# Kernel optimization log

Measured on AMD Instinct MI355X. Metric: run time of the kernel, lower is better.

Reference implementation:

```python
import jax, jax.numpy as jnp
import numpy as np

D = 256
B, S, N = 4, 512, 4


def setup_inputs() -> dict:
    key = jax.random.key(0)
    ks = jax.random.split(key, 24)
    d, dq = D, D // 4
    std = 0.02
    inp = {
        'x':   jax.random.normal(ks[0], (B, S, N, d), jnp.float32),
        'Wq':  jax.random.normal(ks[1], (d, d), jnp.float32) * std,
        'Wk':  jax.random.normal(ks[2], (d, d), jnp.float32) * std,
        'Wv':  jax.random.normal(ks[3], (d, d), jnp.float32) * std,
        'Wg1': jax.random.normal(ks[4], (d, d), jnp.float32) * std,
        'bg1': jnp.zeros((d,), jnp.float32),
        'Wg2': jax.random.normal(ks[5], (d, d), jnp.float32) * std,
        'bg2': jnp.zeros((d,), jnp.float32),
        'We1': jax.random.normal(ks[6], (d, dq), jnp.float32) * std,
        'be1': jnp.zeros((dq,), jnp.float32),
        'We2': jax.random.normal(ks[7], (dq, 1), jnp.float32) * std,
        'be2': jnp.zeros((1,), jnp.float32),
        'Wa1': jax.random.normal(ks[8], (d, dq), jnp.float32) * std,
        'ba1': jnp.zeros((dq,), jnp.float32),
        'Wa2': jax.random.normal(ks[9], (dq, 1), jnp.float32) * std,
        'ba2': jnp.zeros((1,), jnp.float32),
        'Wo':  jax.random.normal(ks[10], (d, d), jnp.float32) * std,
        'bo':  jnp.zeros((d,), jnp.float32),
        'gamma': jnp.ones((d,), jnp.float32),
        'beta':  jnp.zeros((d,), jnp.float32),
    }
    return inp


def reference(x, Wq, Wk, Wv, Wg1, bg1, Wg2, bg2, We1, be1, We2, be2,
              Wa1, ba1, Wa2, ba2, Wo, bo, gamma, beta):
    b, s, n, f = x.shape
    xf = x.reshape(b * n, s, f)  # matches torch .view on contiguous x
    residual = xf

    q = xf @ Wq                                    # [bn, s, d]
    k = xf @ Wk
    v = xf @ Wv
    v_hat = jax.nn.silu(v @ Wg1 + bg1) @ Wg2 + bg2  # value_generator
    eta = jax.nn.sigmoid(jax.nn.silu(xf @ We1 + be1) @ We2 + be2) * 0.1 + 0.01   # [bn, s, 1]
    alpha = jax.nn.sigmoid(jax.nn.silu(xf @ Wa1 + ba1) @ Wa2 + ba2) * 0.5 + 0.5  # [bn, s, 1]

    # F.normalize(k, dim=-1): eps = 1e-12
    kn = k / jnp.maximum(jnp.linalg.norm(k, axis=-1, keepdims=True), 1e-12)

    M0 = jnp.zeros((b * n, f, f), x.dtype)

    def step(M, inp):
        q_t, k_t, v_t, e_t, a_t = inp  # [bn,d],[bn,d],[bn,d],[bn,1],[bn,1]
        out_t = jnp.einsum('bij,bj->bi', M, q_t)
        Mk = jnp.einsum('bij,bj->bi', M, k_t)
        e = e_t[:, :, None]  # [bn,1,1]
        a = a_t[:, :, None]
        # delta rule: M <- a*M - e*(Mk k^T) + e*(v k^T)
        M_new = a * M + e * ((v_t - Mk)[:, :, None] * k_t[:, None, :])
        return M_new, out_t

    seq = (jnp.swapaxes(q, 0, 1), jnp.swapaxes(kn, 0, 1), jnp.swapaxes(v_hat, 0, 1),
           jnp.swapaxes(eta, 0, 1), jnp.swapaxes(alpha, 0, 1))
    M, outs = jax.lax.scan(step, M0, seq)
    out = jnp.swapaxes(outs, 0, 1)  # [bn, s, d]

    y = out @ Wo + bo + residual  # dropout is identity in eval/reference
    mu = jnp.mean(y, axis=-1, keepdims=True)
    var = jnp.var(y, axis=-1, keepdims=True)
    y = (y - mu) / jnp.sqrt(var + 1e-5) * gamma + beta
    return y.reshape(b, s, n, f), M
```

## Files before the change

kernel.cpp:

```cpp
#include <hip/hip_runtime.h>

#define F_ 256
#define S_ 512
#define NH_ 16
#define CCH 32
#define NCH (S_/CCH)
#define KSTR 264
#define KTSTR 36
#define TSTR 40
#define PSTR 17

typedef __attribute__((ext_vector_type(8))) short short8_t;
typedef __attribute__((ext_vector_type(4))) float f32x4;

__device__ __forceinline__ float sigmoid_f(float x) { return 1.0f / (1.0f + __expf(-x)); }

__device__ __forceinline__ ushort f2bf(float x) {
  uint u = __float_as_uint(x);
  u += 0x7FFFu + ((u >> 16) & 1u);
  return (ushort)(u >> 16);
}
__device__ __forceinline__ float bf2f(ushort u) {
  return __uint_as_float((uint)u << 16);
}

template<int CTRL>
__device__ __forceinline__ float dpp_add(float x) {
  int y = __builtin_amdgcn_update_dpp(0, __float_as_int(x), CTRL, 0xf, 0xf, true);
  return x + __int_as_float(y);
}
__device__ __forceinline__ float red8(float x) {
  x = dpp_add<0xB1>(x);
  x = dpp_add<0x4E>(x);
  x = dpp_add<0x141>(x);
  return x;
}

__global__ __launch_bounds__(256) void wconv_k(
    const float* __restrict__ Wq, const float* __restrict__ Wk,
    const float* __restrict__ Wv, const float* __restrict__ Wg1,
    const float* __restrict__ Wg2, const float* __restrict__ Wo,
    const float* __restrict__ We1, const float* __restrict__ Wa1,
    const float* __restrict__ be1, const float* __restrict__ ba1,
    const float* __restrict__ x,
    ushort* __restrict__ Wt, float* __restrict__ beas,
    ushort* __restrict__ xb)
{
  const int blk = blockIdx.x, tid = threadIdx.x;
  if (blk >= 105) {
    const size_t base = (size_t)(blk - 105) * 16384;
    #pragma unroll
    for (int p = 0; p < 16; ++p) {
      const size_t o = base + (size_t)(((p << 8) + tid) << 2);
      const float4 v = *(const float4*)&x[o];
      ushort4 h4;
      h4.x = f2bf(v.x); h4.y = f2bf(v.y); h4.z = f2bf(v.z); h4.w = f2bf(v.w);
      *(ushort4*)&xb[o] = h4;
    }
    return;
  }
  if (blk == 104) {
    if (tid < 64) beas[tid] = be1[tid];
    else if (tid < 128) beas[tid] = ba1[tid - 64];
    return;
  }
  __shared__ float tile[64][65];
  const float* src; int N, k0, n0; size_t dstbase;
  if (blk < 96) {
    const int w = blk >> 4, tl = blk & 15;
    const float* ws_[6] = {Wq, Wk, Wv, Wg1, Wg2, Wo};
    const size_t dstb[6] = {0, 65536, 131072, 229376, 294912, 360448};
    src = ws_[w]; N = 256;
    k0 = (tl >> 2) * 64; n0 = (tl & 3) * 64;
    dstbase = dstb[w];
  } else {
    const int w = (blk - 96) >> 2, tl = (blk - 96) & 3;
    src = w ? Wa1 : We1; N = 64;
    k0 = tl * 64; n0 = 0;
    dstbase = w ? 212992 : 196608;
  }
  #pragma unroll
  for (int p = 0; p < 4; ++p) {
    const int idx = (p << 8) + tid;
    const int r = idx >> 4, c4 = (idx & 15) << 2;
    if (c4 < N) {
      const float4 v = *(const float4*)&src[(size_t)(k0 + r) * N + n0 + c4];
      tile[r][c4 + 0] = v.x; tile[r][c4 + 1] = v.y;
      tile[r][c4 + 2] = v.z; tile[r][c4 + 3] = v.w;
    }
  }
  __syncthreads();
  #pragma unroll
  for (int p = 0; p < 4; ++p) {
    const int idx = (p << 8) + tid;
    const int nl = idx >> 4, kc = (idx & 15) << 2;
    if (nl < ((blk < 96) ? 64 : 64) && (n0 + nl) < ((blk < 96) ? 256 : 64)) {
      ushort4 o;
      o.x = f2bf(tile[kc + 0][nl]); o.y = f2bf(tile[kc + 1][nl]);
      o.z = f2bf(tile[kc + 2][nl]); o.w = f2bf(tile[kc + 3][nl]);
      *(ushort4*)&Wt[dstbase + (size_t)(n0 + nl) * 256 + k0 + kc] = o;
    }
  }
}

__global__ __launch_bounds__(256) void qkve_k(
    const ushort* __restrict__ A, const ushort* __restrict__ Wt,
    const float* __restrict__ beas,
    ushort* __restrict__ qb, float* __restrict__ kf,
    ushort* __restrict__ vb, float* __restrict__ sesa)
{
  __shared__ ushort As[2][64 * 72];
  __shared__ ushort Ws[2][64 * 72];
  const int tid = threadIdx.x;
  const int wv = tid >> 6, l = tid & 63;
  const int ln = l & 15, hi = l >> 4, hi4 = hi << 2, hi8 = hi << 3;
  const int wr = wv >> 1, wc = wv & 1;
  const int row0 = blockIdx.y * 64, col0 = blockIdx.x * 64;
  const int r_ = tid >> 3, c8_ = (tid & 7) << 3;

  short8_t pA[2], pB[2];
  auto loadT = [&](int k0) {
    pA[0] = *(const short8_t*)&A[(size_t)(row0 + r_) * 256 + k0 + c8_];
    pA[1] = *(const short8_t*)&A[(size_t)(row0 + 32 + r_) * 256 + k0 + c8_];
    pB[0] = *(const short8_t*)&Wt[(size_t)(col0 + r_) * 256 + k0 + c8_];
    pB[1] = *(const short8_t*)&Wt[(size_t)(col0 + 32 + r_) * 256 + k0 + c8_];
  };
  auto commitT = [&](int b) {
    *(short8_t*)&As[b][r_ * 72 + c8_] = pA[0];
    *(short8_t*)&As[b][(32 + r_) * 72 + c8_] = pA[1];
    *(short8_t*)&Ws[b][r_ * 72 + c8_] = pB[0];
    *(short8_t*)&Ws[b][(32 + r_) * 72 + c8_] = pB[1];
  };

  f32x4 acc[2][2];
  #pragma unroll
  for (int i = 0; i < 2; ++i)
    #pragma unroll
    for (int j = 0; j < 2; ++j)
      #pragma unroll
      for (int r = 0; r < 4; ++r) acc[i][j][r] = 0.f;

  loadT(0); commitT(0); __syncthreads();
  #pragma unroll
  for (int t = 0; t < 4; ++t) {
    const int b = t & 1;
    if (t < 3) loadT((t + 1) << 6);
    #pragma unroll
    for (int kk = 0; kk < 2; ++kk) {
      short8_t a0 = *(const short8_t*)&As[b][(wr * 32 + ln) * 72 + kk * 32 + hi8];
      short8_t a1 = *(const short8_t*)&As[b][(wr * 32 + 16 + ln) * 72 + kk * 32 + hi8];
      short8_t b0 = *(const short8_t*)&Ws[b][(wc * 32 + ln) * 72 + kk * 32 + hi8];
      short8_t b1 = *(const short8_t*)&Ws[b][(wc * 32 + 16 + ln) * 72 + kk * 32 + hi8];
      acc[0][0] = __builtin_amdgcn_mfma_f32_16x16x32_bf16(a0, b0, acc[0][0], 0, 0, 0);
      acc[0][1] = __builtin_amdgcn_mfma_f32_16x16x32_bf16(a0, b1, acc[0][1], 0, 0, 0);
      acc[1][0] = __builtin_amdgcn_mfma_f32_16x16x32_bf16(a1, b0, acc[1][0], 0, 0, 0);
      acc[1][1] = __builtin_amdgcn_mfma_f32_16x16x32_bf16(a1, b1, acc[1][1], 0, 0, 0);
    }
    if (t < 3) commitT(b ^ 1);
    __syncthreads();
  }

  #pragma unroll
  for (int mi = 0; mi < 2; ++mi)
    #pragma unroll
    for (int ni = 0; ni < 2; ++ni) {
      const int col = col0 + wc * 32 + ni * 16 + ln;
      #pragma unroll
      for (int r = 0; r < 4; ++r) {
        const int row = row0 + wr * 32 + mi * 16 + hi4 + r;
        float vx = acc[mi][ni][r];
        if (col0 < 256)      qb[(size_t)row * 256 + col] = f2bf(vx);
        else if (col0 < 512) kf[(size_t)row * 256 + (col - 256)] = vx;
        else if (col0 < 768) vb[(size_t)row * 256 + (col - 512)] = f2bf(vx);
        else {
          const int cc = col - 768;
          vx += beas[cc];
          vx *= sigmoid_f(vx);
          sesa[(size_t)row * 128 + cc] = vx;
        }
      }
    }
}

__global__ __launch_bounds__(256) void gemm_bf16_k(
    const ushort* __restrict__ A, const ushort* __restrict__ Wt,
    const float* __restrict__ bias, float* __restrict__ Cf,
    ushort* __restrict__ Cb, int act)
{
  __shared__ ushort As[2][64 * 72];
  __shared__ ushort Ws[2][64 * 72];
  const int tid = threadIdx.x;
  const int wv = tid >> 6, l = tid & 63;
  const int ln = l & 15, hi = l >> 4, hi4 = hi << 2, hi8 = hi << 3;
  const int wr = wv >> 1, wc = wv & 1;
  const int row0 = blockIdx.y * 64, col0 = blockIdx.x * 64;
  const int r_ = tid >> 3, c8_ = (tid & 7) << 3;

  short8_t pA[2], pB[2];
  auto loadT = [&](int k0) {
    pA[0] = *(const short8_t*)&A[(size_t)(row0 + r_) * 256 + k0 + c8_];
    pA[1] = *(const short8_t*)&A[(size_t)(row0 + 32 + r_) * 256 + k0 + c8_];
    pB[0] = *(const short8_t*)&Wt[(size_t)(col0 + r_) * 256 + k0 + c8_];
    pB[1] = *(const short8_t*)&Wt[(size_t)(col0 + 32 + r_) * 256 + k0 + c8_];
  };
  auto commitT = [&](int b) {
    *(short8_t*)&As[b][r_ * 72 + c8_] = pA[0];
    *(short8_t*)&As[b][(32 + r_) * 72 + c8_] = pA[1];
    *(short8_t*)&Ws[b][r_ * 72 + c8_] = pB[0];
    *(short8_t*)&Ws[b][(32 + r_) * 72 + c8_] = pB[1];
  };

  f32x4 acc[2][2];
  #pragma unroll
  for (int i = 0; i < 2; ++i)
    #pragma unroll
    for (int j = 0; j < 2; ++j)
      #pragma unroll
      for (int r = 0; r < 4; ++r) acc[i][j][r] = 0.f;

  loadT(0); commitT(0); __syncthreads();
  #pragma unroll
  for (int t = 0; t < 4; ++t) {
    const int b = t & 1;
    if (t < 3) loadT((t + 1) << 6);
    #pragma unroll
    for (int kk = 0; kk < 2; ++kk) {
      short8_t a0 = *(const short8_t*)&As[b][(wr * 32 + ln) * 72 + kk * 32 + hi8];
      short8_t a1 = *(const short8_t*)&As[b][(wr * 32 + 16 + ln) * 72 + kk * 32 + hi8];
      short8_t b0 = *(const short8_t*)&Ws[b][(wc * 32 + ln) * 72 + kk * 32 + hi8];
      short8_t b1 = *(const short8_t*)&Ws[b][(wc * 32 + 16 + ln) * 72 + kk * 32 + hi8];
      acc[0][0] = __builtin_amdgcn_mfma_f32_16x16x32_bf16(a0, b0, acc[0][0], 0, 0, 0);
      acc[0][1] = __builtin_amdgcn_mfma_f32_16x16x32_bf16(a0, b1, acc[0][1], 0, 0, 0);
      acc[1][0] = __builtin_amdgcn_mfma_f32_16x16x32_bf16(a1, b0, acc[1][0], 0, 0, 0);
      acc[1][1] = __builtin_amdgcn_mfma_f32_16x16x32_bf16(a1, b1, acc[1][1], 0, 0, 0);
    }
    if (t < 3) commitT(b ^ 1);
    __syncthreads();
  }

  #pragma unroll
  for (int mi = 0; mi < 2; ++mi)
    #pragma unroll
    for (int ni = 0; ni < 2; ++ni) {
      const int col = col0 + wc * 32 + ni * 16 + ln;
      const float bval = bias ? bias[col] : 0.f;
      #pragma unroll
      for (int r = 0; r < 4; ++r) {
        const int row = row0 + wr * 32 + mi * 16 + hi4 + r;
        float vx = acc[mi][ni][r] + bval;
        if (act == 1) vx = vx * sigmoid_f(vx);
        if (Cf) Cf[(size_t)row * 256 + col] = vx;
        if (Cb) Cb[(size_t)row * 256 + col] = f2bf(vx);
      }
    }
}

__global__ __launch_bounds__(256) void knea_k(
    const float* __restrict__ kf, ushort* __restrict__ kb,
    const float* __restrict__ sesa,
    const float* __restrict__ We2, const float* __restrict__ be2,
    const float* __restrict__ Wa2, const float* __restrict__ ba2,
    float* __restrict__ eta, float* __restrict__ alpha)
{
  const int lane = threadIdx.x & 63;
  const size_t row = ((size_t)blockIdx.x << 2) + (threadIdx.x >> 6);
  {
    const size_t off = row * F_ + ((size_t)lane << 2);
    float4 v = *(const float4*)&kf[off];
    float ss = v.x * v.x + v.y * v.y + v.z * v.z + v.w * v.w;
    #pragma unroll
    for (int m = 1; m < 64; m <<= 1) ss += __shfl_xor(ss, m, 64);
    const float sc = 1.0f / fmaxf(sqrtf(ss), 1e-12f);
    ushort4 o;
    o.x = f2bf(v.x * sc); o.y = f2bf(v.y * sc);
    o.z = f2bf(v.z * sc); o.w = f2bf(v.w * sc);
    *(ushort4*)&kb[off] = o;
  }
  {
    float pe = sesa[row * 128 + lane] * We2[lane];
    float pa = sesa[row * 128 + 64 + lane] * Wa2[lane];
    #pragma unroll
    for (int m = 1; m < 64; m <<= 1) {
      pe += __shfl_xor(pe, m, 64);
      pa += __shfl_xor(pa, m, 64);
    }
    if (lane == 0) {
      eta[row]   = sigmoid_f(pe + be2[0]) * 0.1f + 0.01f;
      alpha[row] = sigmoid_f(pa + ba2[0]) * 0.5f + 0.5f;
    }
  }
}

__global__ __launch_bounds__(256) void ln_k(
    const float* __restrict__ t, const float* __restrict__ x,
    const float* __restrict__ gamma, const float* __restrict__ beta,
    float* __restrict__ y)
{
  const int lane = threadIdx.x & 63;
  const size_t row = ((size_t)blockIdx.x << 2) + (threadIdx.x >> 6);
  const size_t off = row * F_ + ((size_t)lane << 2);
  const float4 tv = *(const float4*)&t[off];
  const float4 xv = *(const float4*)&x[off];
  float4 v = make_float4(tv.x + xv.x, tv.y + xv.y, tv.z + xv.z, tv.w + xv.w);
  float sm = v.x + v.y + v.z + v.w;
  float sq = v.x * v.x + v.y * v.y + v.z * v.z + v.w * v.w;
  #pragma unroll
  for (int m = 1; m < 64; m <<= 1) {
    sm += __shfl_xor(sm, m, 64);
    sq += __shfl_xor(sq, m, 64);
  }
  const float mu  = sm * (1.0f / 256.0f);
  const float var = sq * (1.0f / 256.0f) - mu * mu;
  const float rstd = rsqrtf(var + 1e-5f);
  const float4 g = *(const float4*)&gamma[(size_t)lane << 2];
  const float4 b = *(const float4*)&beta[(size_t)lane << 2];
  float4 o;
  o.x = (v.x - mu) * rstd * g.x + b.x;
  o.y = (v.y - mu) * rstd * g.y + b.y;
  o.z = (v.z - mu) * rstd * g.z + b.z;
  o.w = (v.w - mu) * rstd * g.w + b.w;
  *(float4*)&y[off] = o;
}

__global__ __launch_bounds__(256) void prep_k(
    const ushort* __restrict__ kb, const ushort* __restrict__ qb,
    const float* __restrict__ eta, const float* __restrict__ alpha,
    ushort* __restrict__ Tg, ushort* __restrict__ Gqg, float* __restrict__ Sg,
    ushort* __restrict__ Ktg)
{
  __shared__ ushort K_lds[CCH * KSTR];
  __shared__ ushort Q_lds[CCH * KSTR];
  __shared__ float  G_lds[CCH * CCH];
  __shared__ float  ea[2 * CCH];
  __shared__ float  scal[100];

  const int tid = threadIdx.x;
  const int ch = blockIdx.x, h = blockIdx.y;
  const int t0 = ch * CCH;
  const int l = tid & 63, wv = tid >> 6;
  const int ln = l & 15, hi = l >> 4;
  const int hi8 = hi * 8, hi4 = hi * 4;

  const ushort* kg = kb + (size_t)(h * S_ + t0) * F_;
  const ushort* qg = qb + (size_t)(h * S_ + t0) * F_;
  #pragma unroll
  for (int w = 0; w < 4; ++w) {
    int o = w * 256 + tid; int t = o >> 5, c8 = (o & 31) << 3;
    *(short8_t*)&K_lds[t * KSTR + c8] = *(const short8_t*)&kg[(size_t)t * F_ + c8];
    *(short8_t*)&Q_lds[t * KSTR + c8] = *(const short8_t*)&qg[(size_t)t * F_ + c8];
  }
  if (tid < CCH)            ea[tid] = eta[(size_t)h * S_ + t0 + tid];
  else if (tid < 2 * CCH)   ea[tid] = alpha[(size_t)h * S_ + t0 + tid - CCH];
  __syncthreads();

  {
    const int tt = tid & 31, cl = tid >> 5;
    for (int cp = 0; cp < 32; ++cp) {
      const int c = cp * 8 + cl;
      Ktg[((size_t)h * F_ + c) * S_ + t0 + tt] = K_lds[tt * KSTR + c];
    }
  }

  {
    const int tI = wv >> 1, tJ = wv & 1;
    f32x4 accG = {0.f, 0.f, 0.f, 0.f};
    f32x4 accQ = {0.f, 0.f, 0.f, 0.f};
    #pragma unroll
    for (int ko = 0; ko < 8; ++ko) {
      const int cb = ko * 32 + hi8;
      short8_t bfr = *(const short8_t*)&K_lds[(tJ * 16 + ln) * KSTR + cb];
      short8_t aK  = *(const short8_t*)&K_lds[(tI * 16 + ln) * KSTR + cb];
      short8_t aQ  = *(const short8_t*)&Q_lds[(tI * 16 + ln) * KSTR + cb];
      accG = __builtin_amdgcn_mfma_f32_16x16x32_bf16(aK, bfr, accG, 0, 0, 0);
      accQ = __builtin_amdgcn_mfma_f32_16x16x32_bf16(aQ, bfr, accQ, 0, 0, 0);
    }
    ushort* Gqo = Gqg + (size_t)(h * NCH + ch) * (CCH * CCH);
    #pragma unroll
    for (int r = 0; r < 4; ++r) {
      const int t = tI * 16 + hi4 + r, s = tJ * 16 + ln;
      G_lds[t * CCH + s] = accG[r];
      Gqo[t * CCH + s] = (s < t) ? f2bf(accQ[r]) : (ushort)0;
    }
  }
  if (tid == 0) {
    float gp = 1.f;
    for (int t = 0; t < CCH; ++t) {
      const float a = ea[CCH + t], e = ea[t];
      const float gm = gp * a;
      scal[t]           = e / a;
      scal[CCH + t]     = e / gm;
      scal[2 * CCH + t] = gp;
      gp = gm;
    }
    scal[3 * CCH] = gp;
  }
  __syncthreads();

  {
    const int j = tid >> 3, g = tid & 7;
    float x0 = 0.f, x1 = 0.f, x2 = 0.f, x3 = 0.f;
    ushort* To = Tg + (size_t)(h * NCH + ch) * (CCH * CCH);
    #pragma unroll
    for (int t = 0; t < CCH; ++t) {
      float p = 0.f;
      const f32x4 gr = *(const f32x4*)&G_lds[t * CCH + 4 * g];
      if (4 * g + 0 < t) p += gr[0] * x0;
      if (4 * g + 1 < t) p += gr[1] * x1;
      if (4 * g + 2 < t) p += gr[2] * x2;
      if (4 * g + 3 < t) p += gr[3] * x3;
      const float tot = red8(p);
      const float xt = ((t == j) ? 1.f : 0.f) - scal[t] * tot;
      if (g == (t >> 2)) {
        if ((t & 3) == 0) x0 = xt; else if ((t & 3) == 1) x1 = xt;
        else if ((t & 3) == 2) x2 = xt; else x3 = xt;
      }
      if (g == 0) To[t * CCH + j] = f2bf(xt);
    }
  }
  if (tid < 97) Sg[(size_t)(h * NCH + ch) * 128 + tid] = scal[tid];
}

__global__ __launch_bounds__(256, 1) void scan_chunk_k(
    const ushort* __restrict__ kb, const ushort* __restrict__ qb,
    const ushort* __restrict__ vhb, const ushort* __restrict__ Ktg,
    const ushort* __restrict__ Tg, const ushort* __restrict__ Gqg,
    const float* __restrict__ Sg,
    ushort* __restrict__ outb, float* __restrict__ Mout)
{
  __shared__ ushort K_lds[CCH * KSTR];
  __shared__ ushort Q_lds[CCH * KSTR];
  __shared__ ushort Kt_lds[2][F_ * KTSTR];
  __shared__ ushort M_lds[2][16 * KSTR];
  __shared__ ushort T_lds[CCH * TSTR];
  __shared__ ushort Gq_lds[2][CCH * TSTR];
  __shared__ ushort Wt_lds[16 * TSTR];
  __shared__ ushort R_lds[16 * TSTR];
  __shared__ float  KMp[4 * CCH * PSTR];
  __shared__ float  QM_lds[CCH * PSTR];
  __shared__ ushort V_lds[CCH * 16];
  __shared__ float  scal[2][104];

  const int tid = threadIdx.x;
  const int flat = blockIdx.x;
  const int h = (flat & 7) + ((flat >> 7) << 3);
  const int slice = (flat >> 3) & 15;
  const int r0 = slice * 16;
  const int wv = tid >> 6, l = tid & 63;
  const int ln = l & 15, hi = l >> 4, hi4 = hi << 2, hi8 = hi << 3;

  for (int u = tid; u < 16 * KSTR / 8; u += 256) {
    short8_t z = {0, 0, 0, 0, 0, 0, 0, 0};
    *(short8_t*)&M_lds[0][u * 8] = z;
  }
  f32x4 Mf[4];
  #pragma unroll
  for (int q = 0; q < 4; ++q)
    #pragma unroll
    for (int r = 0; r < 4; ++r) Mf[q][r] = 0.f;

  const ushort* kgh = kb + (size_t)h * S_ * F_;
  const ushort* qgh = qb + (size_t)h * S_ * F_;
  const ushort* kth = Ktg + (size_t)h * F_ * S_;

  short8_t pK[4], pQ[4], pKt[4], pTG;
  ushort pV[2]; float pS = 0.f;

  auto loadchunk = [&](int ch) {
    const int t0 = ch * CCH;
    #pragma unroll
    for (int r = 0; r < 4; ++r) {
      const int idx = (r << 8) + tid;
      const int t = idx >> 5, c8 = (idx & 31) << 3;
      pK[r] = *(const short8_t*)&kgh[(size_t)(t0 + t) * F_ + c8];
      pQ[r] = *(const short8_t*)&qgh[(size_t)(t0 + t) * F_ + c8];
    }
    #pragma unroll
    for (int r = 0; r < 4; ++r) {
      const int idx = (r << 8) + tid;
      const int c = idx >> 2, t8 = (idx & 3) << 3;
      pKt[r] = *(const short8_t*)&kth[(size_t)c * S_ + t0 + t8];
    }
    #pragma unroll
    for (int u = 0; u < 2; ++u) {
      const int e = (u << 8) + tid, t = e >> 4, i = e & 15;
      pV[u] = vhb[(size_t)(h * S_ + t0 + t) * F_ + r0 + i];
    }
    {
      const ushort* Ti = Tg  + (size_t)(h * NCH + ch) * (CCH * CCH);
      const ushort* Gi = Gqg + (size_t)(h * NCH + ch) * (CCH * CCH);
      if (tid < 128) {
        const int t = tid >> 2, c8 = (tid & 3) << 3;
        pTG = *(const short8_t*)&Ti[t * CCH + c8];
      } else {
        const int t = (tid - 128) >> 2, c8 = ((tid - 128) & 3) << 3;
        pTG = *(const short8_t*)&Gi[t * CCH + c8];
      }
    }
    if (tid < 97) pS = Sg[(size_t)(h * NCH + ch) * 128 + tid];
  };

  auto commit = [&](int b) {
    #pragma unroll
    for (int r = 0; r < 4; ++r) {
      const int idx = (r << 8) + tid;
      const int t = idx >> 5, c8 = (idx & 31) << 3;
      *(short8_t*)&K_lds[t * KSTR + c8] = pK[r];
      *(short8_t*)&Q_lds[t * KSTR + c8] = pQ[r];
    }
    #pragma unroll
    for (int r = 0; r < 4; ++r) {
      const int idx = (r << 8) + tid;
      const int c = idx >> 2, t8 = (idx & 3) << 3;
      *(short8_t*)&Kt_lds[b][c * KTSTR + t8] = pKt[r];
    }
    #pragma unroll
    for (int u = 0; u < 2; ++u) V_lds[(u << 8) + tid] = pV[u];
    if (tid < 128) {
      const int t = tid >> 2, c8 = (tid & 3) << 3;
      *(short8_t*)&T_lds[t * TSTR + c8] = pTG;
    } else {
      const int t = (tid - 128) >> 2, c8 = ((tid - 128) & 3) << 3;
      *(short8_t*)&Gq_lds[b][t * TSTR + c8] = pTG;
    }
    if (tid < 97) scal[b][tid] = pS;
  };

  loadchunk(0);
  commit(0);
  __syncthreads();
  int cb = 0;

  for (int ch = 0; ch < NCH; ++ch) {
    const int t0 = ch * CCH;
    const int nb = cb ^ 1;
    if (ch + 1 < NCH) loadchunk(ch + 1);

    {
      const int j0 = wv * 64;
      f32x4 a0v = {0.f, 0.f, 0.f, 0.f};
      f32x4 a1v = {0.f, 0.f, 0.f, 0.f};
      #pragma unroll
      for (int ks = 0; ks < 2; ++ks) {
        const int jc = j0 + ks * 32 + hi8;
        short8_t bm = *(const short8_t*)&M_lds[cb][ln * KSTR + jc];
        short8_t a0 = *(const short8_t*)&K_lds[ln * KSTR + jc];
        short8_t a1 = *(const short8_t*)&K_lds[(16 + ln) * KSTR + jc];
        a0v = __builtin_amdgcn_mfma_f32_16x16x32_bf16(a0, bm, a0v, 0, 0, 0);
        a1v = __builtin_amdgcn_mfma_f32_16x16x32_bf16(a1, bm, a1v, 0, 0, 0);
      }
      #pragma unroll
      for (int r = 0; r < 4; ++r) {
        KMp[wv * (CCH * PSTR) + (hi4 + r) * PSTR + ln] = a0v[r];
        KMp[wv * (CCH * PSTR) + (16 + hi4 + r) * PSTR + ln] = a1v[r];
      }
    }
    __syncthreads();

    if (wv == 0) {
      const int i = l & 15, tg = l >> 4;
      short8_t rv;
      #pragma unroll
      for (int u = 0; u < 8; ++u) {
        const int t = tg * 8 + u;
        const float s = KMp[t * PSTR + i]
                      + KMp[CCH * PSTR + t * PSTR + i]
                      + KMp[2 * CCH * PSTR + t * PSTR + i]
                      + KMp[3 * CCH * PSTR + t * PSTR + i];
        const float rhs = scal[cb][CCH + t] * bf2f(V_lds[t * 16 + i])
                        - scal[cb][t] * s;
        rv[u] = (short)f2bf(rhs);
      }
      *(short8_t*)&R_lds[i * TSTR + tg * 8] = rv;
      #pragma unroll
      for (int I = 0; I < 2; ++I) {
        short8_t a = *(const short8_t*)&T_lds[(I * 16 + ln) * TSTR + hi8];
        short8_t b = *(const short8_t*)&R_lds[ln * TSTR + hi8];
        f32x4 z = {0.f, 0.f, 0.f, 0.f};
        f32x4 d = __builtin_amdgcn_mfma_f32_16x16x32_bf16(a, b, z, 0, 0, 0);
        ushort4 wo;
        wo.x = f2bf(d[0]); wo.y = f2bf(d[1]); wo.z = f2bf(d[2]); wo.w = f2bf(d[3]);
        *(ushort4*)&Wt_lds[ln * TSTR + I * 16 + hi4] = wo;
      }
    } else if (wv >= 2) {
      const int I = wv - 2;
      f32x4 acc = {0.f, 0.f, 0.f, 0.f};
      #pragma unroll
      for (int ko = 0; ko < 8; ++ko) {
        short8_t a = *(const short8_t*)&Q_lds[(I * 16 + ln) * KSTR + ko * 32 + hi8];
        short8_t b = *(const short8_t*)&M_lds[cb][ln * KSTR + ko * 32 + hi8];
        acc = __builtin_amdgcn_mfma_f32_16x16x32_bf16(a, b, acc, 0, 0, 0);
      }
      #pragma unroll
      for (int r = 0; r < 4; ++r)
        QM_lds[(I * 16 + hi4 + r) * PSTR + ln] = acc[r];
    }
    __syncthreads();

    {
      const float gC = scal[cb][3 * CCH];
      short8_t aw = *(const short8_t*)&Wt_lds[ln * TSTR + hi8];
      #pragma unroll
      for (int qq = 0; qq < 4; ++qq) {
        const int jt = wv * 4 + qq;
        short8_t bk = *(const short8_t*)&Kt_lds[cb][(jt * 16 + ln) * KTSTR + hi8];
        f32x4 d = __builtin_amdgcn_mfma_f32_16x16x32_bf16(aw, bk, Mf[qq], 0, 0, 0);
        #pragma unroll
        for (int r = 0; r < 4; ++r) {
          const float nv = gC * d[r];
          Mf[qq][r] = nv;
          M_lds[nb][(hi4 + r) * KSTR + jt * 16 + ln] = f2bf(nv);
        }
      }
    }
    if (wv < 2) {
      const int I = wv;
      short8_t a = *(const short8_t*)&Gq_lds[cb][(I * 16 + ln) * TSTR + hi8];
      short8_t b = *(const short8_t*)&Wt_lds[ln * TSTR + hi8];
      f32x4 z = {0.f, 0.f, 0.f, 0.f};
      f32x4 d = __builtin_amdgcn_mfma_f32_16x16x32_bf16(a, b, z, 0, 0, 0);
      #pragma unroll
      for (int r = 0; r < 4; ++r) {
        const int t = I * 16 + hi4 + r;
        const float ov = scal[cb][2 * CCH + t] * (QM_lds[t * PSTR + ln] + d[r]);
        outb[(size_t)(h * S_ + t0 + t) * F_ + r0 + ln] = f2bf(ov);
      }
    }
    if (ch + 1 < NCH) commit(nb);
    __syncthreads();
    cb = nb;
  }

  #pragma unroll
  for (int qq = 0; qq < 4; ++qq) {
    const int jt = wv * 4 + qq;
    #pragma unroll
    for (int r = 0; r < 4; ++r)
      Mout[((size_t)h * F_ + r0 + hi4 + r) * F_ + jt * 16 + ln] = Mf[qq][r];
  }
}

extern "C" void kernel_launch(void* const* d_in, const int* in_sizes, int n_in,
                              void* d_out, int out_size, void* d_ws, size_t ws_size,
                              hipStream_t stream)
{
  const float* x    = (const float*)d_in[0];
  const float* Wq   = (const float*)d_in[1];
  const float* Wk   = (const float*)d_in[2];
  const float* Wv   = (const float*)d_in[3];
  const float* Wg1  = (const float*)d_in[4];
  const float* bg1  = (const float*)d_in[5];
  const float* Wg2  = (const float*)d_in[6];
  const float* bg2  = (const float*)d_in[7];
  const float* We1  = (const float*)d_in[8];
  const float* be1  = (const float*)d_in[9];
  const float* We2  = (const float*)d_in[10];
  const float* be2  = (const float*)d_in[11];
  const float* Wa1  = (const float*)d_in[12];
  const float* ba1  = (const float*)d_in[13];
  const float* Wa2  = (const float*)d_in[14];
  const float* ba2  = (const float*)d_in[15];
  const float* Wo   = (const float*)d_in[16];
  const float* bo   = (const float*)d_in[17];
  const float* gamma= (const float*)d_in[18];
  const float* beta = (const float*)d_in[19];

  const int Mrows = NH_ * S_;
  const size_t MM = 1048576;
  const size_t NTF = 2 * MM;

  float* ws = (float*)d_ws;
  ushort* xb   = (ushort*)(ws + 0 * MM);
  ushort* outb = (ushort*)(ws + 0 * MM);
  ushort* qb   = (ushort*)(ws + 1 * MM);
  ushort* kb   = (ushort*)(ws + 2 * MM);
  float*  kf   = ws + 3 * MM;
  ushort* t1b  = (ushort*)(ws + 3 * MM);
  ushort* vhb  = (ushort*)(ws + 4 * MM);
  ushort* vb   = (ushort*)(ws + 5 * MM);
  float*  sesa = ws + 6 * MM;
  float*  ytmp = ws + 5 * MM;
  float*  eta  = ws + 7 * MM;
  float*  alpha= eta + Mrows;
  ushort* Tg   = (ushort*)(ws + 7 * MM + 16384);
  ushort* Gqg  = Tg + 262144;
  float*  Sg   = ws + 7 * MM + 16384 + 131072 + 131072;
  ushort* Ktg  = (ushort*)(Sg + 32768);
  ushort* Wt   = Ktg + 2097152;
  float*  beas = (float*)(Wt + 425984);

  dim3 blk(256);

  wconv_k<<<233, blk, 0, stream>>>(Wq, Wk, Wv, Wg1, Wg2, Wo, We1, Wa1,
                                   be1, ba1, x, Wt, beas, xb);

  qkve_k<<<dim3(14, 128), blk, 0, stream>>>(xb, Wt, beas, qb, kf, vb, sesa);

  knea_k<<<Mrows / 4, blk, 0, stream>>>(kf, kb, sesa, We2, be2, Wa2, ba2, eta, alpha);

  gemm_bf16_k<<<dim3(4, 128), blk, 0, stream>>>(vb,  Wt + 229376, bg1, nullptr, t1b, 1);
  gemm_bf16_k<<<dim3(4, 128), blk, 0, stream>>>(t1b, Wt + 294912, bg2, nullptr, vhb, 0);

  prep_k<<<dim3(NCH, NH_), blk, 0, stream>>>(kb, qb, eta, alpha, Tg, Gqg, Sg, Ktg);

  float* yout = (float*)d_out;
  float* Mfin = yout + NTF;
  scan_chunk_k<<<256, blk, 0, stream>>>(kb, qb, vhb, Ktg, Tg, Gqg, Sg, outb, Mfin);

  gemm_bf16_k<<<dim3(4, 128), blk, 0, stream>>>(outb, Wt + 360448, bo, ytmp, nullptr, 0);
  ln_k<<<Mrows / 4, blk, 0, stream>>>(ytmp, x, gamma, beta, yout);
}
```

Before: 101.2 us.

## Double chunk size to 64 in delta-rule scan with blocked triangular solve

Doubles the scan chunk length from 32 to 64, which halves the number of sequential chunk iterations and their barriers in the scan kernel. The 64x64 triangular inverse is never formed. prep_k still emits two 32x32 inverse blocks plus a cross-block coupling matrix C, and the scan applies them as a two-stage blocked forward substitution. The intra-chunk Q·K^T mask becomes 64x64. Double-buffering of Kt/Gq/M in LDS is replaced by a split commit (A/B) into single buffers. This raises per-iteration work, serial wave-0 work and register pressure.

Result: slower. 110.2 us (+8.9%).

```diff
diff --git a/kernel.cpp b/kernel.cpp
--- a/kernel.cpp
+++ b/kernel.cpp
@@ -3,12 +3,12 @@
 #define F_ 256
 #define S_ 512
 #define NH_ 16
-#define CCH 32
+#define CCH 64
 #define NCH (S_/CCH)
 #define KSTR 264
-#define KTSTR 36
-#define TSTR 40
-#define PSTR 17
+#define KT2 72
+#define TST2 40
+#define GST 72
 
 typedef __attribute__((ext_vector_type(8))) short short8_t;
 typedef __attribute__((ext_vector_type(4))) float f32x4;
@@ -94,7 +94,7 @@
   for (int p = 0; p < 4; ++p) {
     const int idx = (p << 8) + tid;
     const int nl = idx >> 4, kc = (idx & 15) << 2;
-    if (nl < ((blk < 96) ? 64 : 64) && (n0 + nl) < ((blk < 96) ? 256 : 64)) {
+    if ((n0 + nl) < ((blk < 96) ? 256 : 64)) {
       ushort4 o;
       o.x = f2bf(tile[kc + 0][nl]); o.y = f2bf(tile[kc + 1][nl]);
       o.z = f2bf(tile[kc + 2][nl]); o.w = f2bf(tile[kc + 3][nl]);
@@ -325,32 +325,43 @@
 __global__ __launch_bounds__(256) void prep_k(
     const ushort* __restrict__ kb, const ushort* __restrict__ qb,
     const float* __restrict__ eta, const float* __restrict__ alpha,
-    ushort* __restrict__ Tg, ushort* __restrict__ Gqg, float* __restrict__ Sg,
-    ushort* __restrict__ Ktg)
+    ushort* __restrict__ Tg, ushort* __restrict__ Gqg, ushort* __restrict__ Cg,
+    float* __restrict__ Sg, ushort* __restrict__ Ktg)
 {
-  __shared__ ushort K_lds[CCH * KSTR];
-  __shared__ ushort Q_lds[CCH * KSTR];
-  __shared__ float  G_lds[CCH * CCH];
-  __shared__ float  ea[2 * CCH];
-  __shared__ float  scal[100];
+  __shared__ ushort K_lds[32 * KSTR];
+  __shared__ ushort Q_lds[32 * KSTR];
+  __shared__ ushort Ko_lds[32 * KSTR];
+  __shared__ float  G_lds[32 * 32];
+  __shared__ float  ea[128];
+  __shared__ float  scal[200];
 
   const int tid = threadIdx.x;
-  const int ch = blockIdx.x, h = blockIdx.y;
-  const int t0 = ch * CCH;
+  const int ch32 = blockIdx.x, h = blockIdx.y;
+  const int ch64 = ch32 >> 1, odd = ch32 & 1;
+  const int t0 = ch32 * 32;
+  const int t064 = ch64 * 64;
   const int l = tid & 63, wv = tid >> 6;
   const int ln = l & 15, hi = l >> 4;
   const int hi8 = hi * 8, hi4 = hi * 4;
 
   const ushort* kg = kb + (size_t)(h * S_ + t0) * F_;
   const ushort* qg = qb + (size_t)(h * S_ + t0) * F_;
+  const ushort* kog = kb + (size_t)(h * S_ + t064) * F_;
   #pragma unroll
   for (int w = 0; w < 4; ++w) {
     int o = w * 256 + tid; int t = o >> 5, c8 = (o & 31) << 3;
     *(short8_t*)&K_lds[t * KSTR + c8] = *(const short8_t*)&kg[(size_t)t * F_ + c8];
     *(short8_t*)&Q_lds[t * KSTR + c8] = *(const short8_t*)&qg[(size_t)t * F_ + c8];
   }
-  if (tid < CCH)            ea[tid] = eta[(size_t)h * S_ + t0 + tid];
-  else if (tid < 2 * CCH)   ea[tid] = alpha[(size_t)h * S_ + t0 + tid - CCH];
+  if (odd) {
+    #pragma unroll
+    for (int w = 0; w < 4; ++w) {
+      int o = w * 256 + tid; int t = o >> 5, c8 = (o & 31) << 3;
+      *(short8_t*)&Ko_lds[t * KSTR + c8] = *(const short8_t*)&kog[(size_t)t * F_ + c8];
+    }
+  }
+  if (tid < 64)        ea[tid] = eta[(size_t)h * S_ + t064 + tid];
+  else if (tid < 128)  ea[tid] = alpha[(size_t)h * S_ + t064 + tid - 64];
   __syncthreads();
 
   {
@@ -361,84 +372,103 @@
     }
   }
 
+  if (tid == 0) {
+    float gp = 1.f;
+    for (int t = 0; t < 64; ++t) {
+      const float a = ea[64 + t], e = ea[t];
+      const float gm = gp * a;
+      scal[t]        = e / a;
+      scal[64 + t]   = e / gm;
+      scal[128 + t]  = gp;
+      gp = gm;
+    }
+    scal[192] = gp;
+  }
+
+  const int tI = wv >> 1, tJ = wv & 1;
+  f32x4 accG = {0.f,0.f,0.f,0.f}, accQ = {0.f,0.f,0.f,0.f};
+  f32x4 accGo = {0.f,0.f,0.f,0.f}, accQo = {0.f,0.f,0.f,0.f};
+  #pragma unroll
+  for (int ko = 0; ko < 8; ++ko) {
+    const int cb = ko * 32 + hi8;
+    short8_t bK = *(const short8_t*)&K_lds[(tJ * 16 + ln) * KSTR + cb];
+    short8_t aK = *(const short8_t*)&K_lds[(tI * 16 + ln) * KSTR + cb];
+    short8_t aQ = *(const short8_t*)&Q_lds[(tI * 16 + ln) * KSTR + cb];
+    accG = __builtin_amdgcn_mfma_f32_16x16x32_bf16(aK, bK, accG, 0, 0, 0);
+    accQ = __builtin_amdgcn_mfma_f32_16x16x32_bf16(aQ, bK, accQ, 0, 0, 0);
+    if (odd) {
+      short8_t bKo = *(const short8_t*)&Ko_lds[(tJ * 16 + ln) * KSTR + cb];
+      accGo = __builtin_amdgcn_mfma_f32_16x16x32_bf16(aK, bKo, accGo, 0, 0, 0);
+      accQo = __builtin_amdgcn_mfma_f32_16x16x32_bf16(aQ, bKo, accQo, 0, 0, 0);
+    }
+  }
   {
-    const int tI = wv >> 1, tJ = wv & 1;
-    f32x4 accG = {0.f, 0.f, 0.f, 0.f};
-    f32x4 accQ = {0.f, 0.f, 0.f, 0.f};
-    #pragma unroll
-    for (int ko = 0; ko < 8; ++ko) {
-      const int cb = ko * 32 + hi8;
-      short8_t bfr = *(const short8_t*)&K_lds[(tJ * 16 + ln) * KSTR + cb];
-      short8_t aK  = *(const short8_t*)&K_lds[(tI * 16 + ln) * KSTR + cb];
-      short8_t aQ  = *(const short8_t*)&Q_lds[(tI * 16 + ln) * KSTR + cb];
-      accG = __builtin_amdgcn_mfma_f32_16x16x32_bf16(aK, bfr, accG, 0, 0, 0);
-      accQ = __builtin_amdgcn_mfma_f32_16x16x32_bf16(aQ, bfr, accQ, 0, 0, 0);
-    }
-    ushort* Gqo = Gqg + (size_t)(h * NCH + ch) * (CCH * CCH);
+    ushort* Gqo = Gqg + (size_t)(h * NCH + ch64) * 4096;
     #pragma unroll
     for (int r = 0; r < 4; ++r) {
       const int t = tI * 16 + hi4 + r, s = tJ * 16 + ln;
-      G_lds[t * CCH + s] = accG[r];
-      Gqo[t * CCH + s] = (s < t) ? f2bf(accQ[r]) : (ushort)0;
-    }
-  }
-  if (tid == 0) {
-    float gp = 1.f;
-    for (int t = 0; t < CCH; ++t) {
-      const float a = ea[CCH + t], e = ea[t];
-      const float gm = gp * a;
-      scal[t]           = e / a;
-      scal[CCH + t]     = e / gm;
-      scal[2 * CCH + t] = gp;
-      gp = gm;
-    }
-    scal[3 * CCH] = gp;
+      G_lds[t * 32 + s] = accG[r];
+      Gqo[(odd * 32 + t) * 64 + odd * 32 + s] = (s < t) ? f2bf(accQ[r]) : (ushort)0;
+      if (odd) Gqo[(32 + t) * 64 + s] = f2bf(accQo[r]);
+      else     Gqo[t * 64 + 32 + s] = 0;
+    }
   }
   __syncthreads();
+
+  if (odd) {
+    ushort* Co = Cg + (size_t)(h * NCH + ch64) * 1024;
+    #pragma unroll
+    for (int r = 0; r < 4; ++r) {
+      const int t = tI * 16 + hi4 + r, s = tJ * 16 + ln;
+      Co[t * 32 + s] = f2bf(scal[32 + t] * accGo[r]);
+    }
+  }
 
   {
     const int j = tid >> 3, g = tid & 7;
     float x0 = 0.f, x1 = 0.f, x2 = 0.f, x3 = 0.f;
-    ushort* To = Tg + (size_t)(h * NCH + ch) * (CCH * CCH);
-    #pragma unroll
-    for (int t = 0; t < CCH; ++t) {
+    ushort* To = Tg + (size_t)(h * 16 + ch32) * 1024;
+    #pragma unroll
+    for (int t = 0; t < 32; ++t) {
       float p = 0.f;
-      const f32x4 gr = *(const f32x4*)&G_lds[t * CCH + 4 * g];
+      const f32x4 gr = *(const f32x4*)&G_lds[t * 32 + 4 * g];
       if (4 * g + 0 < t) p += gr[0] * x0;
       if (4 * g + 1 < t) p += gr[1] * x1;
       if (4 * g + 2 < t) p += gr[2] * x2;
       if (4 * g + 3 < t) p += gr[3] * x3;
       const float tot = red8(p);
-      const float xt = ((t == j) ? 1.f : 0.f) - scal[t] * tot;
+      const float xt = ((t == j) ? 1.f : 0.f) - scal[(odd << 5) + t] * tot;
       if (g == (t >> 2)) {
         if ((t & 3) == 0) x0 = xt; else if ((t & 3) == 1) x1 = xt;
         else if ((t & 3) == 2) x2 = xt; else x3 = xt;
       }
-      if (g == 0) To[t * CCH + j] = f2bf(xt);
-    }
-  }
-  if (tid < 97) Sg[(size_t)(h * NCH + ch) * 128 + tid] = scal[tid];
+      if (g == 0) To[t * 32 + j] = f2bf(xt);
+    }
+  }
+  if (!odd && tid < 193) Sg[(size_t)(h * NCH + ch64) * 256 + tid] = scal[tid];
 }
 
 __global__ __launch_bounds__(256, 1) void scan_chunk_k(
     const ushort* __restrict__ kb, const ushort* __restrict__ qb,
     const ushort* __restrict__ vhb, const ushort* __restrict__ Ktg,
-    const ushort* __restrict__ Tg, const ushort* __restrict__ Gqg,
-    const float* __restrict__ Sg,
+    const ushort* __restrict__ Tg, const ushort* __restrict__ Cg,
+    const ushort* __restrict__ Gqg, const float* __restrict__ Sg,
     ushort* __restrict__ outb, float* __restrict__ Mout)
 {
   __shared__ ushort K_lds[CCH * KSTR];
   __shared__ ushort Q_lds[CCH * KSTR];
-  __shared__ ushort Kt_lds[2][F_ * KTSTR];
-  __shared__ ushort M_lds[2][16 * KSTR];
-  __shared__ ushort T_lds[CCH * TSTR];
-  __shared__ ushort Gq_lds[2][CCH * TSTR];
-  __shared__ ushort Wt_lds[16 * TSTR];
-  __shared__ ushort R_lds[16 * TSTR];
-  __shared__ float  KMp[4 * CCH * PSTR];
-  __shared__ float  QM_lds[CCH * PSTR];
+  __shared__ ushort Kt_lds[F_ * KT2];
+  __shared__ ushort M_lds[16 * KSTR];
+  __shared__ ushort T1_lds[32 * TST2];
+  __shared__ ushort T2_lds[32 * TST2];
+  __shared__ ushort C_lds[32 * TST2];
+  __shared__ ushort Gq_lds[CCH * GST];
+  __shared__ ushort Wt_lds[16 * GST];
+  __shared__ ushort R_lds[16 * GST];
+  __shared__ float  QM_lds[CCH * 17];
+  __shared__ float  KMp[2 * CCH * 17];
   __shared__ ushort V_lds[CCH * 16];
-  __shared__ float  scal[2][104];
+  __shared__ float  scal[200];
 
   const int tid = threadIdx.x;
   const int flat = blockIdx.x;
@@ -448,186 +478,229 @@
   const int wv = tid >> 6, l = tid & 63;
   const int ln = l & 15, hi = l >> 4, hi4 = hi << 2, hi8 = hi << 3;
 
-  for (int u = tid; u < 16 * KSTR / 8; u += 256) {
-    short8_t z = {0, 0, 0, 0, 0, 0, 0, 0};
-    *(short8_t*)&M_lds[0][u * 8] = z;
-  }
-  f32x4 Mf[4];
-  #pragma unroll
-  for (int q = 0; q < 4; ++q)
-    #pragma unroll
-    for (int r = 0; r < 4; ++r) Mf[q][r] = 0.f;
-
   const ushort* kgh = kb + (size_t)h * S_ * F_;
   const ushort* qgh = qb + (size_t)h * S_ * F_;
   const ushort* kth = Ktg + (size_t)h * F_ * S_;
 
-  short8_t pK[4], pQ[4], pKt[4], pTG;
-  ushort pV[2]; float pS = 0.f;
+  short8_t pK[8], pQ[8], pKt[8], pT1, pT2, pC, pGq[2];
+  ushort pV[4]; float pS = 0.f;
 
   auto loadchunk = [&](int ch) {
     const int t0 = ch * CCH;
     #pragma unroll
-    for (int r = 0; r < 4; ++r) {
+    for (int r = 0; r < 8; ++r) {
       const int idx = (r << 8) + tid;
       const int t = idx >> 5, c8 = (idx & 31) << 3;
       pK[r] = *(const short8_t*)&kgh[(size_t)(t0 + t) * F_ + c8];
       pQ[r] = *(const short8_t*)&qgh[(size_t)(t0 + t) * F_ + c8];
     }
     #pragma unroll
-    for (int r = 0; r < 4; ++r) {
+    for (int r = 0; r < 8; ++r) {
       const int idx = (r << 8) + tid;
-      const int c = idx >> 2, t8 = (idx & 3) << 3;
+      const int c = idx >> 3, t8 = (idx & 7) << 3;
       pKt[r] = *(const short8_t*)&kth[(size_t)c * S_ + t0 + t8];
     }
     #pragma unroll
-    for (int u = 0; u < 2; ++u) {
+    for (int u = 0; u < 4; ++u) {
       const int e = (u << 8) + tid, t = e >> 4, i = e & 15;
       pV[u] = vhb[(size_t)(h * S_ + t0 + t) * F_ + r0 + i];
     }
     {
-      const ushort* Ti = Tg  + (size_t)(h * NCH + ch) * (CCH * CCH);
-      const ushort* Gi = Gqg + (size_t)(h * NCH + ch) * (CCH * CCH);
+      const ushort* Tb = Tg + (size_t)(h * 16 + ch * 2) * 1024;
       if (tid < 128) {
         const int t = tid >> 2, c8 = (tid & 3) << 3;
-        pTG = *(const short8_t*)&Ti[t * CCH + c8];
+        pT1 = *(const short8_t*)&Tb[t * 32 + c8];
+        pC  = *(const short8_t*)&Cg[(size_t)(h * NCH + ch) * 1024 + t * 32 + c8];
       } else {
         const int t = (tid - 128) >> 2, c8 = ((tid - 128) & 3) << 3;
-        pTG = *(const short8_t*)&Gi[t * CCH + c8];
-      }
-    }
-    if (tid < 97) pS = Sg[(size_t)(h * NCH + ch) * 128 + tid];
+        pT2 = *(const short8_t*)&Tb[1024 + t * 32 + c8];
+      }
+    }
+    #pragma unroll
+    for (int r = 0; r < 2; ++r) {
+      const int idx = (r << 8) + tid;
+      const int t = idx >> 3, c8 = (idx & 7) << 3;
+      pGq[r] = *(const short8_t*)&Gqg[(size_t)(h * NCH + ch) * 4096 + t * 64 + c8];
+    }
+    if (tid < 193) pS = Sg[(size_t)(h * NCH + ch) * 256 + tid];
   };
 
-  auto commit = [&](int b) {
-    #pragma unroll
-    for (int r = 0; r < 4; ++r) {
+  auto commitA = [&]() {
+    #pragma unroll
+    for (int r = 0; r < 8; ++r) {
       const int idx = (r << 8) + tid;
       const int t = idx >> 5, c8 = (idx & 31) << 3;
       *(short8_t*)&K_lds[t * KSTR + c8] = pK[r];
       *(short8_t*)&Q_lds[t * KSTR + c8] = pQ[r];
     }
     #pragma unroll
-    for (int r = 0; r < 4; ++r) {
-      const int idx = (r << 8) + tid;
-      const int c = idx >> 2, t8 = (idx & 3) << 3;
-      *(short8_t*)&Kt_lds[b][c * KTSTR + t8] = pKt[r];
-    }
-    #pragma unroll
-    for (int u = 0; u < 2; ++u) V_lds[(u << 8) + tid] = pV[u];
+    for (int u = 0; u < 4; ++u) V_lds[(u << 8) + tid] = pV[u];
     if (tid < 128) {
       const int t = tid >> 2, c8 = (tid & 3) << 3;
-      *(short8_t*)&T_lds[t * TSTR + c8] = pTG;
+      *(short8_t*)&T1_lds[t * TST2 + c8] = pT1;
+      *(short8_t*)&C_lds[t * TST2 + c8] = pC;
     } else {
       const int t = (tid - 128) >> 2, c8 = ((tid - 128) & 3) << 3;
-      *(short8_t*)&Gq_lds[b][t * TSTR + c8] = pTG;
-    }
-    if (tid < 97) scal[b][tid] = pS;
+      *(short8_t*)&T2_lds[t * TST2 + c8] = pT2;
+    }
   };
 
+  auto commitB = [&]() {
+    #pragma unroll
+    for (int r = 0; r < 8; ++r) {
+      const int idx = (r << 8) + tid;
+      const int c = idx >> 3, t8 = (idx & 7) << 3;
+      *(short8_t*)&Kt_lds[c * KT2 + t8] = pKt[r];
+    }
+    #pragma unroll
+    for (int r = 0; r < 2; ++r) {
+      const int idx = (r << 8) + tid;
+      const int t = idx >> 3, c8 = (idx & 7) << 3;
+      *(short8_t*)&Gq_lds[t * GST + c8] = pGq[r];
+    }
+    if (tid < 193) scal[tid] = pS;
+  };
+
+  for (int u = tid; u < 16 * KSTR / 8; u += 256) {
+    short8_t z = {0,0,0,0,0,0,0,0};
+    *(short8_t*)&M_lds[u * 8] = z;
+  }
+  f32x4 Mf[4];
+  #pragma unroll
+  for (int q = 0; q < 4; ++q)
+    #pragma unroll
+    for (int r = 0; r < 4; ++r) Mf[q][r] = 0.f;
+
   loadchunk(0);
-  commit(0);
+  commitA();
+  commitB();
   __syncthreads();
-  int cb = 0;
 
   for (int ch = 0; ch < NCH; ++ch) {
     const int t0 = ch * CCH;
-    const int nb = cb ^ 1;
+    if (ch > 0) commitB();
     if (ch + 1 < NCH) loadchunk(ch + 1);
 
+    if (wv < 2) {
+      #pragma unroll
+      for (int tt = 0; tt < 4; ++tt) {
+        f32x4 acc = {0.f,0.f,0.f,0.f};
+        #pragma unroll
+        for (int ks = 0; ks < 4; ++ks) {
+          const int jc = wv * 128 + ks * 32 + hi8;
+          short8_t a = *(const short8_t*)&K_lds[(tt * 16 + ln) * KSTR + jc];
+          short8_t b = *(const short8_t*)&M_lds[ln * KSTR + jc];
+          acc = __builtin_amdgcn_mfma_f32_16x16x32_bf16(a, b, acc, 0, 0, 0);
+        }
+        #pragma unroll
+        for (int r = 0; r < 4; ++r)
+          KMp[wv * (CCH * 17) + (tt * 16 + hi4 + r) * 17 + ln] = acc[r];
+      }
+    } else {
+      #pragma unroll
+      for (int tt = 0; tt < 2; ++tt) {
+        const int t16 = (wv - 2) * 32 + tt * 16;
+        f32x4 acc = {0.f,0.f,0.f,0.f};
+        #pragma unroll
+        for (int ko = 0; ko < 8; ++ko) {
+          short8_t a = *(const short8_t*)&Q_lds[(t16 + ln) * KSTR + ko * 32 + hi8];
+          short8_t b = *(const short8_t*)&M_lds[ln * KSTR + ko * 32 + hi8];
+          acc = __builtin_amdgcn_mfma_f32_16x16x32_bf16(a, b, acc, 0, 0, 0);
+        }
+        #pragma unroll
+        for (int r = 0; r < 4; ++r)
+          QM_lds[(t16 + hi4 + r) * 17 + ln] = acc[r];
+      }
+    }
+    __syncthreads();
+
+    if (wv == 0) {
+      const int i = ln, tg = hi;
+      short8_t rv0, rv1;
+      #pragma unroll
+      for (int u = 0; u < 16; ++u) {
+        const int t = tg * 16 + u;
+        const float s = KMp[t * 17 + i] + KMp[CCH * 17 + t * 17 + i];
+        const float rhs = scal[64 + t] * bf2f(V_lds[t * 16 + i]) - scal[t] * s;
+        if (u < 8) rv0[u] = (short)f2bf(rhs); else rv1[u - 8] = (short)f2bf(rhs);
+      }
+      *(short8_t*)&R_lds[i * GST + tg * 16] = rv0;
+      *(short8_t*)&R_lds[i * GST + tg * 16 + 8] = rv1;
+      #pragma unroll
+      for (int I = 0; I < 2; ++I) {
+        short8_t a = *(const short8_t*)&T1_lds[(I * 16 + ln) * TST2 + hi8];
+        short8_t b = *(const short8_t*)&R_lds[ln * GST + hi8];
+        f32x4 z = {0.f,0.f,0.f,0.f};
+        f32x4 d = __builtin_amdgcn_mfma_f32_16x16x32_bf16(a, b, z, 0, 0, 0);
+        #pragma unroll
+        for (int r = 0; r < 4; ++r)
+          Wt_lds[ln * GST + I * 16 + hi4 + r] = f2bf(d[r]);
+      }
+      #pragma unroll
+      for (int I = 0; I < 2; ++I) {
+        short8_t a = *(const short8_t*)&C_lds[(I * 16 + ln) * TST2 + hi8];
+        short8_t b = *(const short8_t*)&Wt_lds[ln * GST + hi8];
+        f32x4 z = {0.f,0.f,0.f,0.f};
+        f32x4 d = __builtin_amdgcn_mfma_f32_16x16x32_bf16(a, b, z, 0, 0, 0);
+        #pragma unroll
+        for (int r = 0; r < 4; ++r) {
+          const int ad = ln * GST + 32 + I * 16 + hi4 + r;
+          R_lds[ad] = f2bf(bf2f(R_lds[ad]) - d[r]);
+        }
+      }
+      #pragma unroll
+      for (int I = 0; I < 2; ++I) {
+        short8_t a = *(const short8_t*)&T2_lds[(I * 16 + ln) * TST2 + hi8];
+        short8_t b = *(const short8_t*)&R_lds[ln * GST + 32 + hi8];
+        f32x4 z = {0.f,0.f,0.f,0.f};
+        f32x4 d = __builtin_amdgcn_mfma_f32_16x16x32_bf16(a, b, z, 0, 0, 0);
+        #pragma unroll
+        for (int r = 0; r < 4; ++r)
+          Wt_lds[ln * GST + 32 + I * 16 + hi4 + r] = f2bf(d[r]);
+      }
+    }
+    __syncthreads();
+
     {
-      const int j0 = wv * 64;
-      f32x4 a0v = {0.f, 0.f, 0.f, 0.f};
-      f32x4 a1v = {0.f, 0.f, 0.f, 0.f};
-      #pragma unroll
-      for (int ks = 0; ks < 2; ++ks) {
-        const int jc = j0 + ks * 32 + hi8;
-        short8_t bm = *(const short8_t*)&M_lds[cb][ln * KSTR + jc];
-        short8_t a0 = *(const short8_t*)&K_lds[ln * KSTR + jc];
-        short8_t a1 = *(const short8_t*)&K_lds[(16 + ln) * KSTR + jc];
-        a0v = __builtin_amdgcn_mfma_f32_16x16x32_bf16(a0, bm, a0v, 0, 0, 0);
-        a1v = __builtin_amdgcn_mfma_f32_16x16x32_bf16(a1, bm, a1v, 0, 0, 0);
-      }
-      #pragma unroll
-      for (int r = 0; r < 4; ++r) {
-        KMp[wv * (CCH * PSTR) + (hi4 + r) * PSTR + ln] = a0v[r];
-        KMp[wv * (CCH * PSTR) + (16 + hi4 + r) * PSTR + ln] = a1v[r];
-      }
-    }
-    __syncthreads();
-
-    if (wv == 0) {
-      const int i = l & 15, tg = l >> 4;
-      short8_t rv;
-      #pragma unroll
-      for (int u = 0; u < 8; ++u) {
-        const int t = tg * 8 + u;
-        const float s = KMp[t * PSTR + i]
-                      + KMp[CCH * PSTR + t * PSTR + i]
-                      + KMp[2 * CCH * PSTR + t * PSTR + i]
-                      + KMp[3 * CCH * PSTR + t * PSTR + i];
-        const float rhs = scal[cb][CCH + t] * bf2f(V_lds[t * 16 + i])
-                        - scal[cb][t] * s;
-        rv[u] = (short)f2bf(rhs);
-      }
-      *(short8_t*)&R_lds[i * TSTR + tg * 8] = rv;
-      #pragma unroll
-      for (int I = 0; I < 2; ++I) {
-        short8_t a = *(const short8_t*)&T_lds[(I * 16 + ln) * TSTR + hi8];
-        short8_t b = *(const short8_t*)&R_lds[ln * TSTR + hi8];
-        f32x4 z = {0.f, 0.f, 0.f, 0.f};
-        f32x4 d = __builtin_amdgcn_mfma_f32_16x16x32_bf16(a, b, z, 0, 0, 0);
-        ushort4 wo;
-        wo.x = f2bf(d[0]); wo.y = f2bf(d[1]); wo.z = f2bf(d[2]); wo.w = f2bf(d[3]);
-        *(ushort4*)&Wt_lds[ln * TSTR + I * 16 + hi4] = wo;
-      }
-    } else if (wv >= 2) {
-      const int I = wv - 2;
-      f32x4 acc = {0.f, 0.f, 0.f, 0.f};
-      #pragma unroll
-      for (int ko = 0; ko < 8; ++ko) {
-        short8_t a = *(const short8_t*)&Q_lds[(I * 16 + ln) * KSTR + ko * 32 + hi8];
-        short8_t b = *(const short8_t*)&M_lds[cb][ln * KSTR + ko * 32 + hi8];
-        acc = __builtin_amdgcn_mfma_f32_16x16x32_bf16(a, b, acc, 0, 0, 0);
-      }
-      #pragma unroll
-      for (int r = 0; r < 4; ++r)
-        QM_lds[(I * 16 + hi4 + r) * PSTR + ln] = acc[r];
-    }
-    __syncthreads();
-
-    {
-      const float gC = scal[cb][3 * CCH];
-      short8_t aw = *(const short8_t*)&Wt_lds[ln * TSTR + hi8];
+      const float gC = scal[192];
       #pragma unroll
       for (int qq = 0; qq < 4; ++qq) {
         const int jt = wv * 4 + qq;
-        short8_t bk = *(const short8_t*)&Kt_lds[cb][(jt * 16 + ln) * KTSTR + hi8];
-        f32x4 d = __builtin_amdgcn_mfma_f32_16x16x32_bf16(aw, bk, Mf[qq], 0, 0, 0);
+        f32x4 acc = Mf[qq];
+        #pragma unroll
+        for (int kk = 0; kk < 2; ++kk) {
+          short8_t a = *(const short8_t*)&Wt_lds[ln * GST + kk * 32 + hi8];
+          short8_t b = *(const short8_t*)&Kt_lds[(jt * 16 + ln) * KT2 + kk * 32 + hi8];
+          acc = __builtin_amdgcn_mfma_f32_16x16x32_bf16(a, b, acc, 0, 0, 0);
+        }
         #pragma unroll
         for (int r = 0; r < 4; ++r) {
-          const float nv = gC * d[r];
-          Mf[qq][r] = nv;
-          M_lds[nb][(hi4 + r) * KSTR + jt * 16 + ln] = f2bf(nv);
+          Mf[qq][r] = gC * acc[r];
+          M_lds[(hi4 + r) * KSTR + jt * 16 + ln] = f2bf(Mf[qq][r]);
         }
       }
     }
-    if (wv < 2) {
-      const int I = wv;
-      short8_t a = *(const short8_t*)&Gq_lds[cb][(I * 16 + ln) * TSTR + hi8];
-      short8_t b = *(const short8_t*)&Wt_lds[ln * TSTR + hi8];
-      f32x4 z = {0.f, 0.f, 0.f, 0.f};
-      f32x4 d = __builtin_amdgcn_mfma_f32_16x16x32_bf16(a, b, z, 0, 0, 0);
-      #pragma unroll
-      for (int r = 0; r < 4; ++r) {
-        const int t = I * 16 + hi4 + r;
-        const float ov = scal[cb][2 * CCH + t] * (QM_lds[t * PSTR + ln] + d[r]);
-        outb[(size_t)(h * S_ + t0 + t) * F_ + r0 + ln] = f2bf(ov);
-      }
-    }
-    if (ch + 1 < NCH) commit(nb);
+    if (wv >= 2) {
+      #pragma unroll
+      for (int I = 0; I < 2; ++I) {
+        const int t16 = ((wv - 2) * 2 + I) * 16;
+        f32x4 acc = {0.f,0.f,0.f,0.f};
+        #pragma unroll
+        for (int kk = 0; kk < 2; ++kk) {
+          short8_t a = *(const short8_t*)&Gq_lds[(t16 + ln) * GST + kk * 32 + hi8];
+          short8_t b = *(const short8_t*)&Wt_lds[ln * GST + kk * 32 + hi8];
+          acc = __builtin_amdgcn_mfma_f32_16x16x32_bf16(a, b, acc, 0, 0, 0);
+        }
+        #pragma unroll
+        for (int r = 0; r < 4; ++r) {
+          const int t = t16 + hi4 + r;
+          const float ov = scal[128 + t] * (QM_lds[t * 17 + ln] + acc[r]);
+          outb[(size_t)(h * S_ + t0 + t) * F_ + r0 + ln] = f2bf(ov);
+        }
+      }
+    }
+    if (ch + 1 < NCH) commitA();
     __syncthreads();
-    cb = nb;
   }
 
   #pragma unroll
@@ -681,12 +754,14 @@
   float*  ytmp = ws + 5 * MM;
   float*  eta  = ws + 7 * MM;
   float*  alpha= eta + Mrows;
-  ushort* Tg   = (ushort*)(ws + 7 * MM + 16384);
-  ushort* Gqg  = Tg + 262144;
-  float*  Sg   = ws + 7 * MM + 16384 + 131072 + 131072;
-  ushort* Ktg  = (ushort*)(Sg + 32768);
-  ushort* Wt   = Ktg + 2097152;
-  float*  beas = (float*)(Wt + 425984);
+  size_t off = 7 * MM + 16384;
+  ushort* Tg   = (ushort*)(ws + off);  off += 131072;
+  ushort* Gqg  = (ushort*)(ws + off);  off += 262144;
+  ushort* Cg   = (ushort*)(ws + off);  off += 65536;
+  float*  Sg   = ws + off;             off += 32768;
+  ushort* Ktg  = (ushort*)(ws + off);  off += 1048576;
+  ushort* Wt   = (ushort*)(ws + off);  off += 212992;
+  float*  beas = ws + off;
 
   dim3 blk(256);
 
@@ -700,11 +775,11 @@
   gemm_bf16_k<<<dim3(4, 128), blk, 0, stream>>>(vb,  Wt + 229376, bg1, nullptr, t1b, 1);
   gemm_bf16_k<<<dim3(4, 128), blk, 0, stream>>>(t1b, Wt + 294912, bg2, nullptr, vhb, 0);
 
-  prep_k<<<dim3(NCH, NH_), blk, 0, stream>>>(kb, qb, eta, alpha, Tg, Gqg, Sg, Ktg);
+  prep_k<<<dim3(16, NH_), blk, 0, stream>>>(kb, qb, eta, alpha, Tg, Gqg, Cg, Sg, Ktg);
 
   float* yout = (float*)d_out;
   float* Mfin = yout + NTF;
-  scan_chunk_k<<<256, blk, 0, stream>>>(kb, qb, vhb, Ktg, Tg, Gqg, Sg, outb, Mfin);
+  scan_chunk_k<<<256, blk, 0, stream>>>(kb, qb, vhb, Ktg, Tg, Cg, Gqg, Sg, outb, Mfin);
 
   gemm_bf16_k<<<dim3(4, 128), blk, 0, stream>>>(outb, Wt + 360448, bo, ytmp, nullptr, 0);
   ln_k<<<Mrows / 4, blk, 0, stream>>>(ytmp, x, gamma, beta, yout);
```
